# Kernel tuning notes

Measured on AMD Instinct MI355X. Metric: run time of the kernel, lower is better.

The kernel has to match this reference:

```python
import jax, jax.numpy as jnp
import numpy as np

NEG_SLOPE = 0.01  # torch leaky_relu default
EPS = 1e-12      # torch F.normalize default


def _edge_mlp(edge_attr, w1, b1, w2, b2, d_h):
    # Sequential(Linear, ReLU, Linear) -> per-edge weight matrices [E, d_h, d_h]
    h = jax.nn.relu(edge_attr @ w1 + b1)
    return (h @ w2 + b2).reshape(-1, d_h, d_h)


def _nnconv(h, src, dst, w_edge, root, bias, n_nodes):
    # message_j->i = x_j @ Theta(e_ji); aggregate (add) at dst; add root transform + bias
    msg = jnp.einsum('ei,eio->eo', h[src], w_edge)  # [E, d_h]
    agg = jax.ops.segment_sum(msg, dst, num_segments=n_nodes)
    return agg + h @ root + bias


def setup_inputs() -> dict:
    key = jax.random.key(0)
    ks = jax.random.split(key, 20)
    N, E, G = 20000, 200000, 128
    d_node, d_edge, d_h, d_out = 64, 16, 32, 32

    x = jax.random.normal(ks[0], (N, d_node), dtype=jnp.float32)
    edge_index = jax.random.randint(ks[1], (2, E), 0, N, dtype=jnp.int32)
    edge_attr = jax.random.normal(ks[2], (E, d_edge), dtype=jnp.float32)
    batch = jnp.sort(jax.random.randint(ks[3], (N,), 0, G, dtype=jnp.int32))

    def lin(k, fan_in, fan_out):
        kw, kb = jax.random.split(k)
        s = 1.0 / np.sqrt(fan_in)
        w = jax.random.uniform(kw, (fan_in, fan_out), jnp.float32, -s, s)
        b = jax.random.uniform(kb, (fan_out,), jnp.float32, -s, s)
        return w, b

    nfc_w, nfc_b = lin(ks[4], d_node, d_h)
    efc1_w1, efc1_b1 = lin(ks[5], d_edge, d_h)
    efc1_w2, efc1_b2 = lin(ks[6], d_h, d_h * d_h)
    root1 = jax.random.uniform(ks[7], (d_h, d_h), jnp.float32, -1/np.sqrt(d_h), 1/np.sqrt(d_h))
    bias1 = jnp.zeros((d_h,), jnp.float32)
    efc2_w1, efc2_b1 = lin(ks[8], d_edge, d_h)
    efc2_w2, efc2_b2 = lin(ks[9], d_h, d_h * d_h)
    root2 = jax.random.uniform(ks[10], (d_h, d_h), jnp.float32, -1/np.sqrt(d_h), 1/np.sqrt(d_h))
    bias2 = jnp.zeros((d_h,), jnp.float32)
    fc_w, fc_b = lin(ks[11], d_h, d_out)

    return dict(x=x, edge_index=edge_index, edge_attr=edge_attr, batch=batch,
                num_graphs=G,
                nfc_w=nfc_w, nfc_b=nfc_b,
                efc1_w1=efc1_w1, efc1_b1=efc1_b1, efc1_w2=efc1_w2, efc1_b2=efc1_b2,
                root1=root1, bias1=bias1,
                efc2_w1=efc2_w1, efc2_b1=efc2_b1, efc2_w2=efc2_w2, efc2_b2=efc2_b2,
                root2=root2, bias2=bias2,
                fc_w=fc_w, fc_b=fc_b)


def reference(x, edge_index, edge_attr, batch, num_graphs,
              nfc_w, nfc_b,
              efc1_w1, efc1_b1, efc1_w2, efc1_b2, root1, bias1,
              efc2_w1, efc2_b1, efc2_w2, efc2_b2, root2, bias2,
              fc_w, fc_b):
    n_nodes = x.shape[0]
    d_h = nfc_w.shape[1]
    src, dst = edge_index[0], edge_index[1]

    lrelu = lambda v: jax.nn.leaky_relu(v, NEG_SLOPE)
    # dropout(p=0.1) is identity at inference
    h = lrelu(x @ nfc_w + nfc_b)

    w_e1 = _edge_mlp(edge_attr, efc1_w1, efc1_b1, efc1_w2, efc1_b2, d_h)
    h = lrelu(_nnconv(h, src, dst, w_e1, root1, bias1, n_nodes))

    w_e2 = _edge_mlp(edge_attr, efc2_w1, efc2_b1, efc2_w2, efc2_b2, d_h)
    atom_embs = lrelu(_nnconv(h, src, dst, w_e2, root2, bias2, n_nodes))

    pooled = jax.ops.segment_sum(atom_embs, batch, num_segments=num_graphs)  # [G, d_h]
    norm = jnp.linalg.norm(pooled, ord=2, axis=1, keepdims=True)
    pooled = pooled / jnp.maximum(norm, EPS)

    out = pooled @ fc_w + fc_b
    return (out, atom_embs)
```

## Files before the change

### kernel.cpp

```cpp
#include <hip/hip_runtime.h>
#include <stdint.h>

#define NN 20000
#define NE 200000
#define NG 128
#define NWJOBS 3125
#define EGRID 782
#define L2SLICE 819

typedef __attribute__((ext_vector_type(8))) short short8;
typedef __attribute__((ext_vector_type(4))) float f32x4;
typedef __attribute__((ext_vector_type(4))) int   int4v;
typedef __attribute__((ext_vector_type(2))) unsigned int uint2v;

static __device__ __forceinline__ float bf2f(short s) {
    union { unsigned int u; float f; } x;
    x.u = ((unsigned int)(unsigned short)s) << 16;
    return x.f;
}
static __device__ __forceinline__ unsigned short f2bf(float f) {
    unsigned int u = __builtin_bit_cast(unsigned int, f);
    u += 0x7fffu + ((u >> 16) & 1u);
    return (unsigned short)(u >> 16);
}
static __device__ __forceinline__ unsigned int pack2bf(float a, float b) {
    unsigned int u0 = __builtin_bit_cast(unsigned int, a) + 0x8000u;
    unsigned int u1 = __builtin_bit_cast(unsigned int, b) + 0x8000u;
    return __builtin_amdgcn_perm(u1, u0, 0x07060302u);
}
static __device__ __forceinline__ int detect_isbf(const unsigned int* x) {
    unsigned int u = x[threadIdx.x & 63];
    unsigned int el = (u >> 7) & 0xffu;
    unsigned long long bm = __ballot((el >= 100u) && (el <= 140u));
    return __popcll(bm) > 32;
}

__global__ __launch_bounds__(256) void k_prep_all(
    const void* x, const void* nfcw, const void* nfcb,
    const void* root1, const void* bias1,
    const void* w2a, const void* b2a, const void* w2b, const void* b2b,
    const void* w1a, const void* b1a, const void* w1b, const void* b1b,
    const void* ea,
    float* __restrict__ h0, float* __restrict__ aggA, float* __restrict__ aggB,
    short* __restrict__ W2Ta, short* __restrict__ W2Tb,
    short* __restrict__ w1t_ws, float* __restrict__ b1f_ws,
    float* __restrict__ pooled, short* __restrict__ ea_ws) {
    const int isbf = detect_isbf((const unsigned int*)x);
    const int b = blockIdx.x;

    if (b < 2500) {
        __shared__ float wf[64 * 32];
        __shared__ float rf[32 * 32];
        __shared__ float bfs[32];
        __shared__ float rb[32];
        __shared__ float xrow[8][66];
        __shared__ float hrow[8][33];
        for (int i = threadIdx.x; i < 64 * 32; i += 256)
            wf[i] = isbf ? bf2f(((const short*)nfcw)[i]) : ((const float*)nfcw)[i];
        for (int i = threadIdx.x; i < 32 * 32; i += 256)
            rf[i] = isbf ? bf2f(((const short*)root1)[i]) : ((const float*)root1)[i];
        if (threadIdx.x < 32) {
            bfs[threadIdx.x] = isbf ? bf2f(((const short*)nfcb)[threadIdx.x])
                                    : ((const float*)nfcb)[threadIdx.x];
            rb[threadIdx.x]  = isbf ? bf2f(((const short*)bias1)[threadIdx.x])
                                    : ((const float*)bias1)[threadIdx.x];
        }
        int t = b * 256 + threadIdx.x;
        int v = t >> 5, c = t & 31, vl = threadIdx.x >> 5;
        if (isbf) {
            const short* xr = (const short*)x + (size_t)v * 64;
            xrow[vl][c]      = bf2f(xr[c]);
            xrow[vl][32 + c] = bf2f(xr[32 + c]);
        } else {
            const float* xr = (const float*)x + (size_t)v * 64;
            xrow[vl][c]      = xr[c];
            xrow[vl][32 + c] = xr[32 + c];
        }
        __syncthreads();
        float acc = bfs[c];
#pragma unroll
        for (int q = 0; q < 64; ++q) acc += xrow[vl][q] * wf[q * 32 + c];
        float hv = acc > 0.f ? acc : 0.01f * acc;
        h0[t] = hv;
        hrow[vl][c] = hv;
        __syncthreads();
        float a2 = rb[c];
#pragma unroll
        for (int q = 0; q < 32; ++q) a2 += hrow[vl][q] * rf[q * 32 + c];
        aggA[t] = a2;
        return;
    }
    if (b < 4327) {
        const int bb = b - 2500;
        if (bb == 0) {
            for (int i = threadIdx.x; i < NG * 32; i += 256) pooled[i] = 0.f;
        }
        if (bb == 1) {
            for (int i = threadIdx.x; i < 1024; i += 256) {
                int layer = i >> 9, jj = i & 511, c = jj >> 4, q = jj & 15;
                const void* w1p = layer ? w1b : w1a;
                w1t_ws[i] = isbf ? ((const short*)w1p)[q * 32 + c]
                                 : (short)f2bf(((const float*)w1p)[q * 32 + c]);
            }
            for (int i = threadIdx.x; i < 64; i += 256) {
                int layer = i >> 5, c = i & 31;
                const void* b1p = layer ? b1b : b1a;
                b1f_ws[i] = isbf ? bf2f(((const short*)b1p)[c])
                                 : ((const float*)b1p)[c];
            }
        }
        int t = bb * 256 + threadIdx.x;
        if (t < 2 * 32 * 1056) {
            int layer = t / (32 * 1056);
            int r = t - layer * (32 * 1056);
            int o = r / 1056, kp = r - o * 1056;
            const void* w2 = layer ? w2b : w2a;
            const void* b2 = layer ? b2b : b2a;
            int idx; const void* sp;
            if (kp < 1024) { int kk = kp >> 5, i = kp & 31; idx = kk * 1024 + i * 32 + o; sp = w2; }
            else           { int i = kp - 1024;             idx = i * 32 + o;             sp = b2; }
            short v = isbf ? ((const short*)sp)[idx] : (short)f2bf(((const float*)sp)[idx]);
            (layer ? W2Tb : W2Ta)[o * 1056 + kp] = v;
            return;
        }
        int u = t - 2 * 32 * 1056;
        if (u < NE * 2 && !isbf) {
            const float* p = (const float*)ea + (size_t)u * 8;
            f32x4 f0 = *(const f32x4*)p;
            f32x4 f1 = *(const f32x4*)(p + 4);
            union { unsigned int d[4]; short8 v; } o8;
            o8.d[0] = pack2bf(f0[0], f0[1]);
            o8.d[1] = pack2bf(f0[2], f0[3]);
            o8.d[2] = pack2bf(f1[0], f1[1]);
            o8.d[3] = pack2bf(f1[2], f1[3]);
            *(short8*)&ea_ws[(size_t)u * 8] = o8.v;
        }
        return;
    }
    {
        int idx = (b - 4327) * 256 + threadIdx.x;
        if (idx < NN * 32 / 4) {
            f32x4 z = {0.f, 0.f, 0.f, 0.f};
            ((f32x4*)aggB)[idx] = z;
        }
    }
}

__global__ __launch_bounds__(256, 4) void k_edge(
    const float* __restrict__ h_in,
    const short* __restrict__ W2T,
    const short* __restrict__ w1pre,
    const float* __restrict__ b1pre,
    const int* __restrict__ src, const int* __restrict__ dst,
    const short* __restrict__ ea_bf,
    const short* __restrict__ ea_ws,
    const unsigned int* xdet,
    float* agg,
    const int layer2, const void* rootp, const void* biasp) {
    __shared__ __align__(16) short h1l[4 * 32 * 68];

    const int isbf = detect_isbf(xdet);
    const short* eap = isbf ? ea_bf : ea_ws;

    if (layer2) {
        const int base = blockIdx.x * L2SLICE;
        for (int i = threadIdx.x; i < L2SLICE; i += 256) {
            int t = base + i;
            if (t < NN * 32) {
                int v = t >> 5, c = t & 31;
                const float* ar = h_in + (size_t)v * 32;
                float acc = isbf ? bf2f(((const short*)biasp)[c]) : ((const float*)biasp)[c];
#pragma unroll
                for (int q = 0; q < 32; ++q) {
                    float hv = ar[q];
                    hv = hv > 0.f ? hv : 0.01f * hv;
                    float wv = isbf ? bf2f(((const short*)rootp)[q * 32 + c])
                                    : ((const float*)rootp)[q * 32 + c];
                    acc += hv * wv;
                }
                atomicAdd(&agg[t], acc);
            }
        }
    }

    const int lane = threadIdx.x & 63;
    const int wid  = threadIdx.x >> 6;
    const int m    = lane & 15;
    const int quad = lane >> 4;
    const int wb   = wid * (32 * 68);

    const int w = blockIdx.x * 4 + wid;
    if (w >= NWJOBS) return;

    short8 w1lo = {0, 0, 0, 0, 0, 0, 0, 0};
    short8 w1hi = {0, 0, 0, 0, 0, 0, 0, 0};
    if (quad < 2) {
        w1lo = *(const short8*)&w1pre[m * 16 + ((quad & 1) << 3)];
        w1hi = *(const short8*)&w1pre[(m + 16) * 16 + ((quad & 1) << 3)];
    }
    const float b1lo = b1pre[m];
    const float b1hi = b1pre[m + 16];
    const f32x4 zero4 = {0.f, 0.f, 0.f, 0.f};

    const int e0 = w << 6;
    short8 eafc[4];
    f32x4 hs[4][2];
    int4v dv[4];
    {
        int s0[4];
#pragma unroll
        for (int mt = 0; mt < 4; ++mt) {
            eafc[mt] = *(const short8*)&eap[(size_t)(e0 + mt * 16 + m) * 16 + ((quad & 1) << 3)];
            s0[mt] = src[e0 + mt * 16 + m];
            dv[mt] = *(const int4v*)&dst[e0 + mt * 16 + (quad << 2)];
        }
#pragma unroll
        for (int mt = 0; mt < 4; ++mt) {
            const float* hr = h_in + (size_t)s0[mt] * 32 + (quad << 3);
            hs[mt][0] = *(const f32x4*)hr;
            hs[mt][1] = *(const f32x4*)(hr + 4);
        }
    }

#pragma unroll
    for (int mt = 0; mt < 4; ++mt) {
        f32x4 alo = __builtin_amdgcn_mfma_f32_16x16x32_bf16(eafc[mt], w1lo, zero4, 0, 0, 0);
        f32x4 ahi = __builtin_amdgcn_mfma_f32_16x16x32_bf16(eafc[mt], w1hi, zero4, 0, 0, 0);
        float v0 = fmaxf(alo[0] + b1lo, 0.f);
        float v1 = fmaxf(alo[1] + b1lo, 0.f);
        float v2 = fmaxf(alo[2] + b1lo, 0.f);
        float v3 = fmaxf(alo[3] + b1lo, 0.f);
        uint2v dlo; dlo[0] = pack2bf(v0, v1); dlo[1] = pack2bf(v2, v3);
        *(uint2v*)&h1l[wb + m * 68 + (mt << 4) + (quad << 2)] = dlo;
        v0 = fmaxf(ahi[0] + b1hi, 0.f);
        v1 = fmaxf(ahi[1] + b1hi, 0.f);
        v2 = fmaxf(ahi[2] + b1hi, 0.f);
        v3 = fmaxf(ahi[3] + b1hi, 0.f);
        uint2v dhi; dhi[0] = pack2bf(v0, v1); dhi[1] = pack2bf(v2, v3);
        *(uint2v*)&h1l[wb + (m + 16) * 68 + (mt << 4) + (quad << 2)] = dhi;
    }
    __asm volatile("s_waitcnt lgkmcnt(0)" ::: "memory");

    short8 hsbf[4];
#pragma unroll
    for (int mt = 0; mt < 4; ++mt) {
        f32x4 g0 = hs[mt][0], g1 = hs[mt][1];
        if (layer2) {
#pragma unroll
            for (int p = 0; p < 4; ++p) {
                g0[p] = g0[p] > 0.f ? g0[p] : 0.01f * g0[p];
                g1[p] = g1[p] > 0.f ? g1[p] : 0.01f * g1[p];
            }
        }
        union { unsigned int du[4]; short8 v; } a;
        a.du[0] = pack2bf(g0[0], g0[1]);
        a.du[1] = pack2bf(g0[2], g0[3]);
        a.du[2] = pack2bf(g1[0], g1[1]);
        a.du[3] = pack2bf(g1[2], g1[3]);
        hsbf[mt] = a.v;
    }

    const short* wr0 = W2T + m * 1056 + (quad << 3);
    const short* wr1 = W2T + (m + 16) * 1056 + (quad << 3);
    f32x4 acc0[4] = {zero4, zero4, zero4, zero4};
    f32x4 acc1[4] = {zero4, zero4, zero4, zero4};
#pragma unroll
    for (int s = 0; s < 32; ++s) {
        short8 bf0 = *(const short8*)(wr0 + (s << 5));
        short8 bf1 = *(const short8*)(wr1 + (s << 5));
#pragma unroll
        for (int mt = 0; mt < 4; ++mt) {
            uint2v hd = *(const uint2v*)&h1l[wb + s * 68 + (mt << 4) + (quad << 2)];
            f32x4 hv;
            hv[0] = __builtin_bit_cast(float, hd[0] << 16);
            hv[1] = __builtin_bit_cast(float, hd[0] & 0xffff0000u);
            hv[2] = __builtin_bit_cast(float, hd[1] << 16);
            hv[3] = __builtin_bit_cast(float, hd[1] & 0xffff0000u);
            f32x4 u0 = __builtin_amdgcn_mfma_f32_16x16x32_bf16(hsbf[mt], bf0, zero4, 0, 0, 0);
            f32x4 u1 = __builtin_amdgcn_mfma_f32_16x16x32_bf16(hsbf[mt], bf1, zero4, 0, 0, 0);
            acc0[mt] += hv * u0;
            acc1[mt] += hv * u1;
        }
    }
    {
        short8 bf0 = *(const short8*)(wr0 + 1024);
        short8 bf1 = *(const short8*)(wr1 + 1024);
#pragma unroll
        for (int mt = 0; mt < 4; ++mt) {
            acc0[mt] = __builtin_amdgcn_mfma_f32_16x16x32_bf16(hsbf[mt], bf0, acc0[mt], 0, 0, 0);
            acc1[mt] = __builtin_amdgcn_mfma_f32_16x16x32_bf16(hsbf[mt], bf1, acc1[mt], 0, 0, 0);
        }
    }

#pragma unroll
    for (int mt = 0; mt < 4; ++mt) {
#pragma unroll
        for (int r = 0; r < 4; ++r) {
            float* ap = agg + (size_t)dv[mt][r] * 32 + m;
            atomicAdd(ap, acc0[mt][r]);
            atomicAdd(ap + 16, acc1[mt][r]);
        }
    }
}

__global__ __launch_bounds__(256) void k_final_nodes(
    const float* __restrict__ agg, const int* __restrict__ batch,
    const unsigned int* xdet, void* __restrict__ out, float* pooled) {
    const int isbf = detect_isbf(xdet);
    __shared__ float gacc[8][32];
    __shared__ int g0s;
    ((float*)gacc)[threadIdx.x] = 0.f;
    if (threadIdx.x == 0) g0s = batch[blockIdx.x * 8];
    __syncthreads();
    int t = blockIdx.x * 256 + threadIdx.x;
    float v = agg[t];
    v = v > 0.f ? v : 0.01f * v;
    if (isbf) ((short*)out)[4096 + t] = (short)f2bf(v);
    else      ((float*)out)[4096 + t] = v;
    int g = batch[t >> 5];
    int rel = g - g0s;
    int c = t & 31;
    if (rel < 8) atomicAdd(&gacc[rel][c], v);
    else         atomicAdd(&pooled[g * 32 + c], v);
    __syncthreads();
    {
        int gi = threadIdx.x >> 5, cc = threadIdx.x & 31;
        float s = gacc[gi][cc];
        if (s != 0.f) atomicAdd(&pooled[(g0s + gi) * 32 + cc], s);
    }
}

__global__ __launch_bounds__(64) void k_graph_out(
    const float* __restrict__ pooled, const void* fcw, const void* fcb,
    const unsigned int* xdet, void* __restrict__ out) {
    const int isbf = detect_isbf(xdet);
    int g = blockIdx.x;
    int t = threadIdx.x;
    __shared__ float pn[32];
    if (t < 32) {
        float p = pooled[g * 32 + t];
        float sq = p * p;
#pragma unroll
        for (int o = 16; o > 0; o >>= 1) sq += __shfl_xor(sq, o, 64);
        float inv = 1.0f / fmaxf(sqrtf(sq), 1e-12f);
        pn[t] = p * inv;
    }
    __syncthreads();
    if (t < 32) {
        float acc = isbf ? bf2f(((const short*)fcb)[t]) : ((const float*)fcb)[t];
#pragma unroll
        for (int q = 0; q < 32; ++q) {
            float wv = isbf ? bf2f(((const short*)fcw)[q * 32 + t])
                            : ((const float*)fcw)[q * 32 + t];
            acc += pn[q] * wv;
        }
        if (isbf) ((short*)out)[g * 32 + t] = (short)f2bf(acc);
        else      ((float*)out)[g * 32 + t] = acc;
    }
}

extern "C" void kernel_launch(void* const* d_in, const int* in_sizes, int n_in,
                              void* d_out, int out_size, void* d_ws, size_t ws_size,
                              hipStream_t stream) {
    (void)in_sizes; (void)n_in; (void)out_size; (void)ws_size;
    const void* x     = d_in[0];
    const int*  eidx  = (const int*)d_in[1];
    const void* ea    = d_in[2];
    const int*  batch = (const int*)d_in[3];
    const void* nfcw  = d_in[5];
    const void* nfcb  = d_in[6];
    const void* e1w1  = d_in[7];
    const void* e1b1  = d_in[8];
    const void* e1w2  = d_in[9];
    const void* e1b2  = d_in[10];
    const void* root1 = d_in[11];
    const void* bias1 = d_in[12];
    const void* e2w1  = d_in[13];
    const void* e2b1  = d_in[14];
    const void* e2w2  = d_in[15];
    const void* e2b2  = d_in[16];
    const void* root2 = d_in[17];
    const void* bias2 = d_in[18];
    const void* fcw   = d_in[19];
    const void* fcb   = d_in[20];
    const unsigned int* xdet = (const unsigned int*)x;

    char* ws = (char*)d_ws;
    float* h0     = (float*)ws; ws += (size_t)NN * 32 * 4;
    float* aggA   = (float*)ws; ws += (size_t)NN * 32 * 4;
    float* aggB   = (float*)ws; ws += (size_t)NN * 32 * 4;
    short* W2T1   = (short*)ws; ws += 32 * 1056 * 2;
    short* W2T2   = (short*)ws; ws += 32 * 1056 * 2;
    short* w1t_ws = (short*)ws; ws += 1024 * 2;
    float* b1f_ws = (float*)ws; ws += 64 * 4;
    float* pooled = (float*)ws; ws += NG * 32 * 4;
    short* ea_ws  = (short*)ws; ws += (size_t)NE * 16 * 2;

    const int* srcp = eidx;
    const int* dstp = eidx + NE;

    k_prep_all<<<4952, 256, 0, stream>>>(
        x, nfcw, nfcb, root1, bias1,
        e1w2, e1b2, e2w2, e2b2, e1w1, e1b1, e2w1, e2b1, ea,
        h0, aggA, aggB, W2T1, W2T2, w1t_ws, b1f_ws, pooled, ea_ws);

    k_edge<<<EGRID, 256, 0, stream>>>(h0, W2T1, w1t_ws, b1f_ws, srcp, dstp,
                                      (const short*)ea, ea_ws, xdet, aggA,
                                      0, nullptr, nullptr);
    k_edge<<<EGRID, 256, 0, stream>>>(aggA, W2T2, w1t_ws + 512, b1f_ws + 32, srcp, dstp,
                                      (const short*)ea, ea_ws, xdet, aggB,
                                      1, root2, bias2);
    k_final_nodes<<<(NN * 32 + 255) / 256, 256, 0, stream>>>(aggB, batch, xdet, d_out, pooled);
    k_graph_out<<<NG, 64, 0, stream>>>(pooled, fcw, fcb, xdet, d_out);
}
```

Baseline: 222.5 us.

## Fuse final node pass with graph output and prefetch W2T fragments in edge loop

Replaces the two tail kernels (per-node leaky-relu plus atomic pooling, then per-graph normalize and FC) with a single per-graph kernel. Each block finds its node range in the sorted batch array by binary search and reduces the sum in shared memory, so the global pooled buffer, its zeroing and the atomics are gone. The edge kernel also software-pipelines its W2T fragment loads four steps ahead through a register ring. The cost is that the tail now runs on only 128 blocks, each walking about 150 nodes serially, and the prefetch ring uses more registers.

New measurement: 218.5 us. No clear change (-1.8%).

```diff
diff --git a/kernel.cpp b/kernel.cpp
--- a/kernel.cpp
+++ b/kernel.cpp
@@ -44,7 +44,7 @@
     float* __restrict__ h0, float* __restrict__ aggA, float* __restrict__ aggB,
     short* __restrict__ W2Ta, short* __restrict__ W2Tb,
     short* __restrict__ w1t_ws, float* __restrict__ b1f_ws,
-    float* __restrict__ pooled, short* __restrict__ ea_ws) {
+    short* __restrict__ ea_ws) {
     const int isbf = detect_isbf((const unsigned int*)x);
     const int b = blockIdx.x;
 
@@ -92,9 +92,6 @@
     }
     if (b < 4327) {
         const int bb = b - 2500;
-        if (bb == 0) {
-            for (int i = threadIdx.x; i < NG * 32; i += 256) pooled[i] = 0.f;
-        }
         if (bb == 1) {
             for (int i = threadIdx.x; i < 1024; i += 256) {
                 int layer = i >> 9, jj = i & 511, c = jj >> 4, q = jj & 15;
@@ -264,31 +261,40 @@
     const short* wr1 = W2T + (m + 16) * 1056 + (quad << 3);
     f32x4 acc0[4] = {zero4, zero4, zero4, zero4};
     f32x4 acc1[4] = {zero4, zero4, zero4, zero4};
-#pragma unroll
-    for (int s = 0; s < 32; ++s) {
-        short8 bf0 = *(const short8*)(wr0 + (s << 5));
-        short8 bf1 = *(const short8*)(wr1 + (s << 5));
-#pragma unroll
-        for (int mt = 0; mt < 4; ++mt) {
-            uint2v hd = *(const uint2v*)&h1l[wb + s * 68 + (mt << 4) + (quad << 2)];
-            f32x4 hv;
-            hv[0] = __builtin_bit_cast(float, hd[0] << 16);
-            hv[1] = __builtin_bit_cast(float, hd[0] & 0xffff0000u);
-            hv[2] = __builtin_bit_cast(float, hd[1] << 16);
-            hv[3] = __builtin_bit_cast(float, hd[1] & 0xffff0000u);
-            f32x4 u0 = __builtin_amdgcn_mfma_f32_16x16x32_bf16(hsbf[mt], bf0, zero4, 0, 0, 0);
-            f32x4 u1 = __builtin_amdgcn_mfma_f32_16x16x32_bf16(hsbf[mt], bf1, zero4, 0, 0, 0);
-            acc0[mt] += hv * u0;
-            acc1[mt] += hv * u1;
-        }
-    }
-    {
-        short8 bf0 = *(const short8*)(wr0 + 1024);
-        short8 bf1 = *(const short8*)(wr1 + 1024);
-#pragma unroll
-        for (int mt = 0; mt < 4; ++mt) {
-            acc0[mt] = __builtin_amdgcn_mfma_f32_16x16x32_bf16(hsbf[mt], bf0, acc0[mt], 0, 0, 0);
-            acc1[mt] = __builtin_amdgcn_mfma_f32_16x16x32_bf16(hsbf[mt], bf1, acc1[mt], 0, 0, 0);
+    short8 q0[4], q1[4];
+#pragma unroll
+    for (int p = 0; p < 4; ++p) {
+        q0[p] = *(const short8*)(wr0 + (p << 5));
+        q1[p] = *(const short8*)(wr1 + (p << 5));
+    }
+#pragma unroll
+    for (int s = 0; s < 33; ++s) {
+        short8 bf0 = q0[s & 3];
+        short8 bf1 = q1[s & 3];
+        if (s + 4 < 33) {
+            q0[s & 3] = *(const short8*)(wr0 + ((s + 4) << 5));
+            q1[s & 3] = *(const short8*)(wr1 + ((s + 4) << 5));
+        }
+        if (s < 32) {
+#pragma unroll
+            for (int mt = 0; mt < 4; ++mt) {
+                uint2v hd = *(const uint2v*)&h1l[wb + s * 68 + (mt << 4) + (quad << 2)];
+                f32x4 hv;
+                hv[0] = __builtin_bit_cast(float, hd[0] << 16);
+                hv[1] = __builtin_bit_cast(float, hd[0] & 0xffff0000u);
+                hv[2] = __builtin_bit_cast(float, hd[1] << 16);
+                hv[3] = __builtin_bit_cast(float, hd[1] & 0xffff0000u);
+                f32x4 u0 = __builtin_amdgcn_mfma_f32_16x16x32_bf16(hsbf[mt], bf0, zero4, 0, 0, 0);
+                f32x4 u1 = __builtin_amdgcn_mfma_f32_16x16x32_bf16(hsbf[mt], bf1, zero4, 0, 0, 0);
+                acc0[mt] += hv * u0;
+                acc1[mt] += hv * u1;
+            }
+        } else {
+#pragma unroll
+            for (int mt = 0; mt < 4; ++mt) {
+                acc0[mt] = __builtin_amdgcn_mfma_f32_16x16x32_bf16(hsbf[mt], bf0, acc0[mt], 0, 0, 0);
+                acc1[mt] = __builtin_amdgcn_mfma_f32_16x16x32_bf16(hsbf[mt], bf1, acc1[mt], 0, 0, 0);
+            }
         }
     }
 
@@ -303,50 +309,50 @@
     }
 }
 
-__global__ __launch_bounds__(256) void k_final_nodes(
+__global__ __launch_bounds__(256) void k_final(
     const float* __restrict__ agg, const int* __restrict__ batch,
-    const unsigned int* xdet, void* __restrict__ out, float* pooled) {
+    const unsigned int* xdet, void* __restrict__ out,
+    const void* fcw, const void* fcb) {
     const int isbf = detect_isbf(xdet);
+    const int g = blockIdx.x;
+    __shared__ int srange[2];
     __shared__ float gacc[8][32];
-    __shared__ int g0s;
-    ((float*)gacc)[threadIdx.x] = 0.f;
-    if (threadIdx.x == 0) g0s = batch[blockIdx.x * 8];
+    __shared__ float pn[32];
+    if (threadIdx.x < 2) {
+        int target = g + (int)threadIdx.x;
+        int lo = 0, hi = NN;
+        while (lo < hi) {
+            int mid = (lo + hi) >> 1;
+            if (batch[mid] < target) lo = mid + 1; else hi = mid;
+        }
+        srange[threadIdx.x] = lo;
+    }
     __syncthreads();
-    int t = blockIdx.x * 256 + threadIdx.x;
-    float v = agg[t];
-    v = v > 0.f ? v : 0.01f * v;
-    if (isbf) ((short*)out)[4096 + t] = (short)f2bf(v);
-    else      ((float*)out)[4096 + t] = v;
-    int g = batch[t >> 5];
-    int rel = g - g0s;
-    int c = t & 31;
-    if (rel < 8) atomicAdd(&gacc[rel][c], v);
-    else         atomicAdd(&pooled[g * 32 + c], v);
+    const int ns = srange[0], ne = srange[1];
+    const int c = threadIdx.x & 31;
+    float psum = 0.f;
+    for (int idx = ns * 32 + threadIdx.x; idx < ne * 32; idx += 256) {
+        float v = agg[idx];
+        v = v > 0.f ? v : 0.01f * v;
+        if (isbf) ((short*)out)[4096 + idx] = (short)f2bf(v);
+        else      ((float*)out)[4096 + idx] = v;
+        psum += v;
+    }
+    gacc[threadIdx.x >> 5][c] = psum;
     __syncthreads();
-    {
-        int gi = threadIdx.x >> 5, cc = threadIdx.x & 31;
-        float s = gacc[gi][cc];
-        if (s != 0.f) atomicAdd(&pooled[(g0s + gi) * 32 + cc], s);
-    }
-}
-
-__global__ __launch_bounds__(64) void k_graph_out(
-    const float* __restrict__ pooled, const void* fcw, const void* fcb,
-    const unsigned int* xdet, void* __restrict__ out) {
-    const int isbf = detect_isbf(xdet);
-    int g = blockIdx.x;
-    int t = threadIdx.x;
-    __shared__ float pn[32];
-    if (t < 32) {
-        float p = pooled[g * 32 + t];
+    if (threadIdx.x < 32) {
+        float p = 0.f;
+#pragma unroll
+        for (int r = 0; r < 8; ++r) p += gacc[r][threadIdx.x];
         float sq = p * p;
 #pragma unroll
         for (int o = 16; o > 0; o >>= 1) sq += __shfl_xor(sq, o, 64);
         float inv = 1.0f / fmaxf(sqrtf(sq), 1e-12f);
-        pn[t] = p * inv;
+        pn[threadIdx.x] = p * inv;
     }
     __syncthreads();
-    if (t < 32) {
+    if (threadIdx.x < 32) {
+        const int t = threadIdx.x;
         float acc = isbf ? bf2f(((const short*)fcb)[t]) : ((const float*)fcb)[t];
 #pragma unroll
         for (int q = 0; q < 32; ++q) {
@@ -393,7 +399,6 @@
     short* W2T2   = (short*)ws; ws += 32 * 1056 * 2;
     short* w1t_ws = (short*)ws; ws += 1024 * 2;
     float* b1f_ws = (float*)ws; ws += 64 * 4;
-    float* pooled = (float*)ws; ws += NG * 32 * 4;
     short* ea_ws  = (short*)ws; ws += (size_t)NE * 16 * 2;
 
     const int* srcp = eidx;
@@ -402,7 +407,7 @@
     k_prep_all<<<4952, 256, 0, stream>>>(
         x, nfcw, nfcb, root1, bias1,
         e1w2, e1b2, e2w2, e2b2, e1w1, e1b1, e2w1, e2b1, ea,
-        h0, aggA, aggB, W2T1, W2T2, w1t_ws, b1f_ws, pooled, ea_ws);
+        h0, aggA, aggB, W2T1, W2T2, w1t_ws, b1f_ws, ea_ws);
 
     k_edge<<<EGRID, 256, 0, stream>>>(h0, W2T1, w1t_ws, b1f_ws, srcp, dstp,
                                       (const short*)ea, ea_ws, xdet, aggA,
@@ -410,6 +415,5 @@
     k_edge<<<EGRID, 256, 0, stream>>>(aggA, W2T2, w1t_ws + 512, b1f_ws + 32, srcp, dstp,
                                       (const short*)ea, ea_ws, xdet, aggB,
                                       1, root2, bias2);
-    k_final_nodes<<<(NN * 32 + 255) / 256, 256, 0, stream>>>(aggB, batch, xdet, d_out, pooled);
-    k_graph_out<<<NG, 64, 0, stream>>>(pooled, fcw, fcb, xdet, d_out);
-}
+    k_final<<<NG, 256, 0, stream>>>(aggB, batch, xdet, d_out, fcw, fcb);
+}
```
